# Kernel optimization log

Hardware: AMD Instinct MI355X
Metric: run time of the kernel (lower is better)

Reference implementation:

```python
import jax, jax.numpy as jnp
import numpy as np

DIST_THRESHOLD = 900.0  # distance_threshold from __init__
NO_CODE_ID = -1         # no_code_id from __init__


def setup_inputs() -> dict:
    key = jax.random.key(0)
    k1, k2 = jax.random.split(key)
    x = jax.random.normal(k1, (4, 2048, 512), dtype=jnp.float32)      # [b, n, d] tokens
    codes = jax.random.normal(k2, (16384, 512), dtype=jnp.float32)    # [c, d] full codebook
    return {"x": x, "codes": codes}


def reference(x, codes):
    x2 = jnp.sum(x * x, axis=-1, keepdims=True)            # [b, n, 1]
    c2 = jnp.sum(codes * codes, axis=-1)                   # [c]
    xc = jnp.einsum('bnd,cd->bnc', x, codes)               # [b, n, c] (the compute-heavy GEMM)
    dist_sq = jnp.maximum(x2 + c2 - 2.0 * xc, 0.0)         # clamp tiny negatives, like cdist

    within = jnp.any(dist_sq <= DIST_THRESHOLD, axis=-1)   # [b, n]
    nn_ids = jnp.argmin(dist_sq, axis=-1)                  # [b, n]
    ids = jnp.where(within, nn_ids, NO_CODE_ID)            # tokens outside threshold -> no_code_id
    return ids
```

## Files before the change

### kernel.cpp

```cpp
#include <hip/hip_runtime.h>


#define NTOK   8192
#define NCODES 16384
#define DDIM   512
#define NCHUNK 8
#define CHUNK  2048
#define DIST_THR 900.0f

typedef unsigned short u16;
typedef _Float16 half8 __attribute__((ext_vector_type(8)));
typedef float    f32x4 __attribute__((ext_vector_type(4)));

__device__ __forceinline__ void conv_body(const float* __restrict__ src,
                                          u16* __restrict__ dh,
                                          u16* __restrict__ dl, int c) {
    int r = c & 15, q = (c >> 4) & 3, g = (c >> 6) & 7, kit = (c >> 9) & 15;
    int tile = c >> 13;
    int row = tile * 128 + g * 16 + r;
    int k = kit * 32 + q * 8;
    const float* p = src + (size_t)row * DDIM + k;
    float4 v0 = *(const float4*)p;
    float4 v1 = *(const float4*)(p + 4);
    float vv[8] = {v0.x, v0.y, v0.z, v0.w, v1.x, v1.y, v1.z, v1.w};
    u16 hs[8], ls[8];
    #pragma unroll
    for (int j = 0; j < 8; ++j) {
        float sv = vv[j] * 16.0f;
        _Float16 h = (_Float16)sv;
        float hf = (float)h;
        _Float16 l = (_Float16)(sv - hf);
        union { _Float16 f; u16 u; } uh, ul;
        uh.f = h; ul.f = l;
        hs[j] = uh.u; ls[j] = ul.u;
    }
    uint4 H, L;
    H.x = hs[0] | ((unsigned)hs[1] << 16); H.y = hs[2] | ((unsigned)hs[3] << 16);
    H.z = hs[4] | ((unsigned)hs[5] << 16); H.w = hs[6] | ((unsigned)hs[7] << 16);
    L.x = ls[0] | ((unsigned)ls[1] << 16); L.y = ls[2] | ((unsigned)ls[3] << 16);
    L.z = ls[4] | ((unsigned)ls[5] << 16); L.w = ls[6] | ((unsigned)ls[7] << 16);
    *(uint4*)(dh + (size_t)c * 8) = H;
    *(uint4*)(dl + (size_t)c * 8) = L;
}

__global__ __launch_bounds__(256) void nn_prep(const float* __restrict__ x,
                                               const float* __restrict__ codes,
                                               u16* __restrict__ xh, u16* __restrict__ xl,
                                               u16* __restrict__ ch, u16* __restrict__ cl,
                                               float* __restrict__ c2) {
    int b = blockIdx.x;
    if (b < 2048) {
        conv_body(x, xh, xl, b * 256 + threadIdx.x);
    } else if (b < 6144) {
        conv_body(codes, ch, cl, (b - 2048) * 256 + threadIdx.x);
    } else {
        int w = threadIdx.x >> 6;
        int lane = threadIdx.x & 63;
        int c = (b - 6144) * 4 + w;
        const float* p = codes + (size_t)c * DDIM + lane * 8;
        float4 v0 = *(const float4*)p;
        float4 v1 = *(const float4*)(p + 4);
        float s = v0.x*v0.x + v0.y*v0.y + v0.z*v0.z + v0.w*v0.w
                + v1.x*v1.x + v1.y*v1.y + v1.z*v1.z + v1.w*v1.w;
        #pragma unroll
        for (int off = 32; off > 0; off >>= 1) s += __shfl_down(s, off);
        if (lane == 0) c2[c] = s;
    }
}

__global__ __launch_bounds__(512, 2) void nn_gemm(const u16* __restrict__ xh,
                                                  const u16* __restrict__ xl,
                                                  const u16* __restrict__ chh,
                                                  const u16* __restrict__ cll,
                                                  const float* __restrict__ c2,
                                                  float* __restrict__ pmin,
                                                  int* __restrict__ pid) {
    __shared__ __align__(16) char smem[131072];
    const int tid = threadIdx.x;
    const int lane = tid & 63;
    const int wave = tid >> 6;
    const int wm = wave & 3;
    const int wn = wave >> 2;
    const int mtile = blockIdx.x >> 3;
    const int chunk = blockIdx.x & 7;
    const int m0 = mtile * 256;

    const int plane = wave >> 1;
    const int tsub  = wave & 1;
    const bool isA = (plane < 2);
    const u16* gbase;
    if (plane == 0)      gbase = xh  + ((size_t)(mtile * 2 + tsub) * 16) * 4096;
    else if (plane == 1) gbase = xl  + ((size_t)(mtile * 2 + tsub) * 16) * 4096;
    else if (plane == 2) gbase = chh + ((size_t)(chunk * 16 + tsub) * 16) * 4096;
    else                 gbase = cll + ((size_t)(chunk * 16 + tsub) * 16) * 4096;
    gbase += lane * 8;
    const int ldsoff = wave * 8192;

    float mv[16];
    int   mi[16];
    #pragma unroll
    for (int s = 0; s < 16; ++s) { mv[s] = 3.4e38f; mi[s] = 0; }

    f32x4 acc[4][8];
    #pragma unroll
    for (int i = 0; i < 4; ++i)
        #pragma unroll
        for (int j = 0; j < 8; ++j) acc[i][j] = (f32x4)0.0f;

    auto stage = [&](int it2) {
        int kit2 = it2 & 15, nt2 = it2 >> 4;
        size_t off = (size_t)(isA ? kit2 : nt2 * 32 + kit2) * 4096;
        const u16* src = gbase + off;
        char* dst = smem + (size_t)(it2 & 1) * 65536 + ldsoff;
        #pragma unroll
        for (int s = 0; s < 8; ++s)
            __builtin_amdgcn_global_load_lds(
                (const __attribute__((address_space(1))) void*)(src + s * 512),
                (__attribute__((address_space(3))) void*)(dst + s * 1024),
                16, 0, 0);
    };

    stage(0);
    for (int it = 0; it < 128; ++it) {
        if (it < 127) {
            stage(it + 1);
            asm volatile("s_waitcnt vmcnt(8)\n\ts_barrier" ::: "memory");
        } else {
            asm volatile("s_waitcnt vmcnt(0)\n\ts_barrier" ::: "memory");
        }

        const char* cur = smem + (size_t)(it & 1) * 65536;
        half8 ah[4], al[4];
        #pragma unroll
        for (int i = 0; i < 4; ++i) {
            int g = wm * 4 + i;
            ah[i] = *(const half8*)(cur +         g * 1024 + lane * 16);
            al[i] = *(const half8*)(cur + 16384 + g * 1024 + lane * 16);
        }
        #pragma unroll
        for (int j = 0; j < 8; ++j) {
            int g = wn * 8 + j;
            half8 bh = *(const half8*)(cur + 32768 + g * 1024 + lane * 16);
            half8 bl = *(const half8*)(cur + 49152 + g * 1024 + lane * 16);
            #pragma unroll
            for (int i = 0; i < 4; ++i) {
                acc[i][j] = __builtin_amdgcn_mfma_f32_16x16x32_f16(ah[i], bh, acc[i][j], 0, 0, 0);
                acc[i][j] = __builtin_amdgcn_mfma_f32_16x16x32_f16(ah[i], bl, acc[i][j], 0, 0, 0);
                acc[i][j] = __builtin_amdgcn_mfma_f32_16x16x32_f16(al[i], bh, acc[i][j], 0, 0, 0);
            }
        }

        if ((it & 15) == 15) {
            int nt = it >> 4;
            #pragma unroll
            for (int j = 0; j < 8; ++j) {
                int ncol = nt * 256 + wn * 128 + j * 16 + (lane & 15);
                int gid = chunk * CHUNK + ncol;
                float cv = c2[gid];
                #pragma unroll
                for (int i = 0; i < 4; ++i)
                    #pragma unroll
                    for (int r = 0; r < 4; ++r) {
                        float s = fmaf(acc[i][j][r], -0.0078125f, cv);
                        int slot = i * 4 + r;
                        if (s < mv[slot]) { mv[slot] = s; mi[slot] = gid; }
                    }
            }
            #pragma unroll
            for (int i = 0; i < 4; ++i)
                #pragma unroll
                for (int j = 0; j < 8; ++j) acc[i][j] = (f32x4)0.0f;
        }
        asm volatile("s_barrier" ::: "memory");
    }

    #pragma unroll
    for (int off = 1; off < 16; off <<= 1) {
        #pragma unroll
        for (int s = 0; s < 16; ++s) {
            float ov = __shfl_xor(mv[s], off);
            int   oi = __shfl_xor(mi[s], off);
            if (ov < mv[s] || (ov == mv[s] && oi < mi[s])) { mv[s] = ov; mi[s] = oi; }
        }
    }
    if ((lane & 15) == 0) {
        #pragma unroll
        for (int i = 0; i < 4; ++i)
            #pragma unroll
            for (int r = 0; r < 4; ++r) {
                int row = wm * 64 + i * 16 + (lane >> 4) * 4 + r;
                int2 e;
                e.x = __float_as_int(mv[i * 4 + r]);
                e.y = mi[i * 4 + r];
                *(int2*)(smem + (wn * 256 + row) * 8) = e;
            }
    }
    __syncthreads();
    if (tid < 256) {
        int2 e0 = *(const int2*)(smem + tid * 8);
        int2 e1 = *(const int2*)(smem + (256 + tid) * 8);
        float v0 = __int_as_float(e0.x), v1 = __int_as_float(e1.x);
        float bv = v0; int bi = e0.y;
        if (v1 < bv || (v1 == bv && e1.y < bi)) { bv = v1; bi = e1.y; }
        pmin[(size_t)(m0 + tid) * NCHUNK + chunk] = bv;
        pid [(size_t)(m0 + tid) * NCHUNK + chunk] = bi;
    }
}

__global__ __launch_bounds__(256) void nn_fin(const float* __restrict__ x,
                                              const float* __restrict__ pmin,
                                              const int* __restrict__ pid,
                                              int* __restrict__ out) {
    int w = threadIdx.x >> 6;
    int lane = threadIdx.x & 63;
    int t = blockIdx.x * 4 + w;
    const float* p = x + (size_t)t * DDIM + lane * 8;
    float4 v0 = *(const float4*)p;
    float4 v1 = *(const float4*)(p + 4);
    float s = v0.x*v0.x + v0.y*v0.y + v0.z*v0.z + v0.w*v0.w
            + v1.x*v1.x + v1.y*v1.y + v1.z*v1.z + v1.w*v1.w;
    #pragma unroll
    for (int off = 32; off > 0; off >>= 1) s += __shfl_down(s, off);
    if (lane == 0) {
        const float* pm = pmin + (size_t)t * NCHUNK;
        const int*   pi = pid  + (size_t)t * NCHUNK;
        float bv = pm[0]; int bi = pi[0];
        #pragma unroll
        for (int c = 1; c < NCHUNK; ++c) {
            float v = pm[c]; int id = pi[c];
            if (v < bv || (v == bv && id < bi)) { bv = v; bi = id; }
        }
        float mind = s + bv;
        out[t] = (mind <= DIST_THR) ? bi : -1;
    }
}

extern "C" void kernel_launch(void* const* d_in, const int* in_sizes, int n_in,
                              void* d_out, int out_size, void* d_ws, size_t ws_size,
                              hipStream_t stream) {
    const float* x     = (const float*)d_in[0];
    const float* codes = (const float*)d_in[1];
    int* out = (int*)d_out;

    char* ws = (char*)d_ws;
    u16*   xh   = (u16*)(ws);
    u16*   xl   = (u16*)(ws + 8388608);
    u16*   chh  = (u16*)(ws + 16777216);
    u16*   cll  = (u16*)(ws + 33554432);
    float* c2   = (float*)(ws + 50331648);
    float* pmin = (float*)(ws + 50397184);
    int*   pid  = (int*)  (ws + 50659328);

    nn_prep<<<10240, 256, 0, stream>>>(x, codes, xh, xl, chh, cll, c2);
    nn_gemm<<<32 * NCHUNK, 512, 0, stream>>>(xh, xl, chh, cll, c2, pmin, pid);
    nn_fin<<<NTOK / 4, 256, 0, stream>>>(x, pmin, pid, out);
}
```

Measured before the change: 409.0 us.

## Interleave LDS reads and MFMA clusters with barriers and priority scheduling

Restructures the main K-loop so B fragments are read from LDS in pairs and each pair's MFMA cluster runs in a fenced block under raised wave priority. Waves are kept in lockstep with extra barriers. The prefetch of the next stage is issued after the first LDS reads, and the wait on the global load moves to the end of the iteration. The aim is to overlap LDS traffic and global-to-LDS loads with MFMA execution, similar to ping-pong scheduling. The cost is many more barriers per iteration, which may add synchronization stalls.

Result: no change. 406.8 us (-0.6%).

```diff
diff --git a/kernel.cpp b/kernel.cpp
--- a/kernel.cpp
+++ b/kernel.cpp
@@ -121,33 +121,63 @@
     };
 
     stage(0);
+    asm volatile("s_waitcnt vmcnt(0)\n\ts_barrier" ::: "memory");
+
     for (int it = 0; it < 128; ++it) {
-        if (it < 127) {
-            stage(it + 1);
-            asm volatile("s_waitcnt vmcnt(8)\n\ts_barrier" ::: "memory");
-        } else {
-            asm volatile("s_waitcnt vmcnt(0)\n\ts_barrier" ::: "memory");
-        }
-
         const char* cur = smem + (size_t)(it & 1) * 65536;
         half8 ah[4], al[4];
+
         #pragma unroll
         for (int i = 0; i < 4; ++i) {
             int g = wm * 4 + i;
             ah[i] = *(const half8*)(cur +         g * 1024 + lane * 16);
             al[i] = *(const half8*)(cur + 16384 + g * 1024 + lane * 16);
         }
-        #pragma unroll
-        for (int j = 0; j < 8; ++j) {
-            int g = wn * 8 + j;
-            half8 bh = *(const half8*)(cur + 32768 + g * 1024 + lane * 16);
-            half8 bl = *(const half8*)(cur + 49152 + g * 1024 + lane * 16);
+        half8 bh0 = *(const half8*)(cur + 32768 + (wn * 8 + 0) * 1024 + lane * 16);
+        half8 bl0 = *(const half8*)(cur + 49152 + (wn * 8 + 0) * 1024 + lane * 16);
+        half8 bh1 = *(const half8*)(cur + 32768 + (wn * 8 + 1) * 1024 + lane * 16);
+        half8 bl1 = *(const half8*)(cur + 49152 + (wn * 8 + 1) * 1024 + lane * 16);
+        if (it < 127) stage(it + 1);
+        asm volatile("s_barrier" ::: "memory");
+        asm volatile("s_waitcnt lgkmcnt(0)" ::: "memory");
+        __builtin_amdgcn_sched_barrier(0);
+        __builtin_amdgcn_s_setprio(1);
+        #pragma unroll
+        for (int i = 0; i < 4; ++i) {
+            acc[i][0] = __builtin_amdgcn_mfma_f32_16x16x32_f16(ah[i], bh0, acc[i][0], 0, 0, 0);
+            acc[i][0] = __builtin_amdgcn_mfma_f32_16x16x32_f16(ah[i], bl0, acc[i][0], 0, 0, 0);
+            acc[i][0] = __builtin_amdgcn_mfma_f32_16x16x32_f16(al[i], bh0, acc[i][0], 0, 0, 0);
+            acc[i][1] = __builtin_amdgcn_mfma_f32_16x16x32_f16(ah[i], bh1, acc[i][1], 0, 0, 0);
+            acc[i][1] = __builtin_amdgcn_mfma_f32_16x16x32_f16(ah[i], bl1, acc[i][1], 0, 0, 0);
+            acc[i][1] = __builtin_amdgcn_mfma_f32_16x16x32_f16(al[i], bh1, acc[i][1], 0, 0, 0);
+        }
+        __builtin_amdgcn_s_setprio(0);
+        __builtin_amdgcn_sched_barrier(0);
+        asm volatile("s_barrier" ::: "memory");
+
+        #pragma unroll
+        for (int p = 1; p < 4; ++p) {
+            const int j0 = 2 * p, j1 = 2 * p + 1;
+            half8 bhA = *(const half8*)(cur + 32768 + (wn * 8 + j0) * 1024 + lane * 16);
+            half8 blA = *(const half8*)(cur + 49152 + (wn * 8 + j0) * 1024 + lane * 16);
+            half8 bhB = *(const half8*)(cur + 32768 + (wn * 8 + j1) * 1024 + lane * 16);
+            half8 blB = *(const half8*)(cur + 49152 + (wn * 8 + j1) * 1024 + lane * 16);
+            asm volatile("s_barrier" ::: "memory");
+            asm volatile("s_waitcnt lgkmcnt(0)" ::: "memory");
+            __builtin_amdgcn_sched_barrier(0);
+            __builtin_amdgcn_s_setprio(1);
             #pragma unroll
             for (int i = 0; i < 4; ++i) {
-                acc[i][j] = __builtin_amdgcn_mfma_f32_16x16x32_f16(ah[i], bh, acc[i][j], 0, 0, 0);
-                acc[i][j] = __builtin_amdgcn_mfma_f32_16x16x32_f16(ah[i], bl, acc[i][j], 0, 0, 0);
-                acc[i][j] = __builtin_amdgcn_mfma_f32_16x16x32_f16(al[i], bh, acc[i][j], 0, 0, 0);
+                acc[i][j0] = __builtin_amdgcn_mfma_f32_16x16x32_f16(ah[i], bhA, acc[i][j0], 0, 0, 0);
+                acc[i][j0] = __builtin_amdgcn_mfma_f32_16x16x32_f16(ah[i], blA, acc[i][j0], 0, 0, 0);
+                acc[i][j0] = __builtin_amdgcn_mfma_f32_16x16x32_f16(al[i], bhA, acc[i][j0], 0, 0, 0);
+                acc[i][j1] = __builtin_amdgcn_mfma_f32_16x16x32_f16(ah[i], bhB, acc[i][j1], 0, 0, 0);
+                acc[i][j1] = __builtin_amdgcn_mfma_f32_16x16x32_f16(ah[i], blB, acc[i][j1], 0, 0, 0);
+                acc[i][j1] = __builtin_amdgcn_mfma_f32_16x16x32_f16(al[i], bhB, acc[i][j1], 0, 0, 0);
             }
+            __builtin_amdgcn_s_setprio(0);
+            __builtin_amdgcn_sched_barrier(0);
+            if (p < 3) asm volatile("s_barrier" ::: "memory");
         }
 
         if ((it & 15) == 15) {
@@ -171,7 +201,7 @@
                 #pragma unroll
                 for (int j = 0; j < 8; ++j) acc[i][j] = (f32x4)0.0f;
         }
-        asm volatile("s_barrier" ::: "memory");
+        asm volatile("s_waitcnt vmcnt(0)\n\ts_barrier" ::: "memory");
     }
 
     #pragma unroll
```

## Load A operands directly from global and stage only B through LDS

Applied to the files above, without the earlier changes.

The x tiles (A hi/lo planes) are now read by each wave straight from global memory into registers, and only the codebook tiles are staged into LDS by all eight waves. This halves shared memory per block and removes the trailing barrier per iteration, with the prefetch of the next B stage issued after the A loads. The cost is that A is re-read from global/L2 every iteration by each wave, and the barrier now waits on vmcnt(0), which exposes global latency more than the old vmcnt(8) double-buffered wait did.

After: 438.1 us. 1.07x slower.

```diff
diff --git a/kernel.cpp b/kernel.cpp
--- a/kernel.cpp
+++ b/kernel.cpp
@@ -75,7 +75,7 @@
                                                   const float* __restrict__ c2,
                                                   float* __restrict__ pmin,
                                                   int* __restrict__ pid) {
-    __shared__ __align__(16) char smem[131072];
+    __shared__ __align__(16) char smem[65536];
     const int tid = threadIdx.x;
     const int lane = tid & 63;
     const int wave = tid >> 6;
@@ -85,21 +85,22 @@
     const int chunk = blockIdx.x & 7;
     const int m0 = mtile * 256;
 
-    const int plane = wave >> 1;
-    const int tsub  = wave & 1;
-    const bool isA = (plane < 2);
-    const u16* gbase;
-    if (plane == 0)      gbase = xh  + ((size_t)(mtile * 2 + tsub) * 16) * 4096;
-    else if (plane == 1) gbase = xl  + ((size_t)(mtile * 2 + tsub) * 16) * 4096;
-    else if (plane == 2) gbase = chh + ((size_t)(chunk * 16 + tsub) * 16) * 4096;
-    else                 gbase = cll + ((size_t)(chunk * 16 + tsub) * 16) * 4096;
-    gbase += lane * 8;
-    const int ldsoff = wave * 8192;
+    const u16* abase_h = xh + (size_t)(mtile * 2 + (wm >> 1)) * 65536
+                            + (size_t)((wm & 1) * 4) * 512 + lane * 8;
+    const u16* abase_l = xl + (size_t)(mtile * 2 + (wm >> 1)) * 65536
+                            + (size_t)((wm & 1) * 4) * 512 + lane * 8;
+
+    const int q = wave >> 2;
+    const int s = wave & 3;
+    const u16* bsrc = q ? cll : chh;
+    const u16* bgbase = bsrc + (size_t)(chunk * 16 + (s >> 1)) * 65536
+                             + (size_t)(s & 1) * 2048 + lane * 8;
+    const int bldsoff = q * 16384 + (s >> 1) * 8192 + (s & 1) * 4096 + lane * 16;
 
     float mv[16];
     int   mi[16];
     #pragma unroll
-    for (int s = 0; s < 16; ++s) { mv[s] = 3.4e38f; mi[s] = 0; }
+    for (int t = 0; t < 16; ++t) { mv[t] = 3.4e38f; mi[t] = 0; }
 
     f32x4 acc[4][8];
     #pragma unroll
@@ -109,39 +110,36 @@
 
     auto stage = [&](int it2) {
         int kit2 = it2 & 15, nt2 = it2 >> 4;
-        size_t off = (size_t)(isA ? kit2 : nt2 * 32 + kit2) * 4096;
-        const u16* src = gbase + off;
-        char* dst = smem + (size_t)(it2 & 1) * 65536 + ldsoff;
-        #pragma unroll
-        for (int s = 0; s < 8; ++s)
+        const u16* src = bgbase + (size_t)nt2 * 131072 + (size_t)kit2 * 4096;
+        char* dst = smem + (it2 & 1) * 32768 + bldsoff;
+        #pragma unroll
+        for (int jj = 0; jj < 4; ++jj)
             __builtin_amdgcn_global_load_lds(
-                (const __attribute__((address_space(1))) void*)(src + s * 512),
-                (__attribute__((address_space(3))) void*)(dst + s * 1024),
+                (const __attribute__((address_space(1))) void*)(src + jj * 512),
+                (__attribute__((address_space(3))) void*)(dst + jj * 1024),
                 16, 0, 0);
     };
 
     stage(0);
     for (int it = 0; it < 128; ++it) {
-        if (it < 127) {
-            stage(it + 1);
-            asm volatile("s_waitcnt vmcnt(8)\n\ts_barrier" ::: "memory");
-        } else {
-            asm volatile("s_waitcnt vmcnt(0)\n\ts_barrier" ::: "memory");
-        }
-
-        const char* cur = smem + (size_t)(it & 1) * 65536;
+        asm volatile("s_waitcnt vmcnt(0)\n\ts_barrier" ::: "memory");
+
+        const char* cur = smem + (it & 1) * 32768;
+        const int kit = it & 15;
+
         half8 ah[4], al[4];
         #pragma unroll
         for (int i = 0; i < 4; ++i) {
-            int g = wm * 4 + i;
-            ah[i] = *(const half8*)(cur +         g * 1024 + lane * 16);
-            al[i] = *(const half8*)(cur + 16384 + g * 1024 + lane * 16);
-        }
+            ah[i] = *(const half8*)(abase_h + (size_t)kit * 4096 + i * 512);
+            al[i] = *(const half8*)(abase_l + (size_t)kit * 4096 + i * 512);
+        }
+        if (it < 127) stage(it + 1);
+
         #pragma unroll
         for (int j = 0; j < 8; ++j) {
             int g = wn * 8 + j;
-            half8 bh = *(const half8*)(cur + 32768 + g * 1024 + lane * 16);
-            half8 bl = *(const half8*)(cur + 49152 + g * 1024 + lane * 16);
+            half8 bh = *(const half8*)(cur +         g * 1024 + lane * 16);
+            half8 bl = *(const half8*)(cur + 16384 + g * 1024 + lane * 16);
             #pragma unroll
             for (int i = 0; i < 4; ++i) {
                 acc[i][j] = __builtin_amdgcn_mfma_f32_16x16x32_f16(ah[i], bh, acc[i][j], 0, 0, 0);
@@ -161,9 +159,9 @@
                 for (int i = 0; i < 4; ++i)
                     #pragma unroll
                     for (int r = 0; r < 4; ++r) {
-                        float s = fmaf(acc[i][j][r], -0.0078125f, cv);
+                        float sc = fmaf(acc[i][j][r], -0.0078125f, cv);
                         int slot = i * 4 + r;
-                        if (s < mv[slot]) { mv[slot] = s; mi[slot] = gid; }
+                        if (sc < mv[slot]) { mv[slot] = sc; mi[slot] = gid; }
                     }
             }
             #pragma unroll
@@ -171,16 +169,15 @@
                 #pragma unroll
                 for (int j = 0; j < 8; ++j) acc[i][j] = (f32x4)0.0f;
         }
-        asm volatile("s_barrier" ::: "memory");
     }
 
     #pragma unroll
     for (int off = 1; off < 16; off <<= 1) {
         #pragma unroll
-        for (int s = 0; s < 16; ++s) {
-            float ov = __shfl_xor(mv[s], off);
-            int   oi = __shfl_xor(mi[s], off);
-            if (ov < mv[s] || (ov == mv[s] && oi < mi[s])) { mv[s] = ov; mi[s] = oi; }
+        for (int t = 0; t < 16; ++t) {
+            float ov = __shfl_xor(mv[t], off);
+            int   oi = __shfl_xor(mi[t], off);
+            if (ov < mv[t] || (ov == mv[t] && oi < mi[t])) { mv[t] = ov; mi[t] = oi; }
         }
     }
     if ((lane & 15) == 0) {
```

## Switch GEMM to 32x32x16 MFMA with per-tile argmin reduction into LDS

Applied to the files above, without the earlier changes.

Replaces the 16x16x32 f16 MFMA tiling with 32x32x16 MFMA, relaying out the converted fp16 hi/lo planes so each lane feeds the larger instruction, and halves LDS fragment reads per MFMA. Because the 32x32 accumulator holds 32 row slots per lane, the running argmin no longer lives in registers. It is reduced across lanes at every N-tile boundary and merged into a new LDS table. This cuts MFMA issue and LDS traffic but adds a shuffle reduction and LDS read-modify-write per N-tile, plus extra LDS space that may affect occupancy.

New measurement: 538.2 us. 1.32x slower.

```diff
diff --git a/kernel.cpp b/kernel.cpp
--- a/kernel.cpp
+++ b/kernel.cpp
@@ -10,15 +10,17 @@
 
 typedef unsigned short u16;
 typedef _Float16 half8 __attribute__((ext_vector_type(8)));
-typedef float    f32x4 __attribute__((ext_vector_type(4)));
+typedef float    f32x4  __attribute__((ext_vector_type(4)));
+typedef float    f32x16 __attribute__((ext_vector_type(16)));
 
 __device__ __forceinline__ void conv_body(const float* __restrict__ src,
                                           u16* __restrict__ dh,
                                           u16* __restrict__ dl, int c) {
-    int r = c & 15, q = (c >> 4) & 3, g = (c >> 6) & 7, kit = (c >> 9) & 15;
+    int L = c & 63, f = (c >> 6) & 7, kit = (c >> 9) & 15;
     int tile = c >> 13;
-    int row = tile * 128 + g * 16 + r;
-    int k = kit * 32 + q * 8;
+    int g = f >> 1, ks = f & 1;
+    int row = tile * 128 + g * 32 + (L & 31);
+    int k = kit * 32 + ks * 16 + (L >> 5) * 8;
     const float* p = src + (size_t)row * DDIM + k;
     float4 v0 = *(const float4*)p;
     float4 v1 = *(const float4*)(p + 4);
@@ -30,17 +32,17 @@
         _Float16 h = (_Float16)sv;
         float hf = (float)h;
         _Float16 l = (_Float16)(sv - hf);
-        union { _Float16 f; u16 u; } uh, ul;
-        uh.f = h; ul.f = l;
+        union { _Float16 f16; u16 u; } uh, ul;
+        uh.f16 = h; ul.f16 = l;
         hs[j] = uh.u; ls[j] = ul.u;
     }
-    uint4 H, L;
-    H.x = hs[0] | ((unsigned)hs[1] << 16); H.y = hs[2] | ((unsigned)hs[3] << 16);
-    H.z = hs[4] | ((unsigned)hs[5] << 16); H.w = hs[6] | ((unsigned)hs[7] << 16);
-    L.x = ls[0] | ((unsigned)ls[1] << 16); L.y = ls[2] | ((unsigned)ls[3] << 16);
-    L.z = ls[4] | ((unsigned)ls[5] << 16); L.w = ls[6] | ((unsigned)ls[7] << 16);
+    uint4 H, Lo;
+    H.x  = hs[0] | ((unsigned)hs[1] << 16); H.y  = hs[2] | ((unsigned)hs[3] << 16);
+    H.z  = hs[4] | ((unsigned)hs[5] << 16); H.w  = hs[6] | ((unsigned)hs[7] << 16);
+    Lo.x = ls[0] | ((unsigned)ls[1] << 16); Lo.y = ls[2] | ((unsigned)ls[3] << 16);
+    Lo.z = ls[4] | ((unsigned)ls[5] << 16); Lo.w = ls[6] | ((unsigned)ls[7] << 16);
     *(uint4*)(dh + (size_t)c * 8) = H;
-    *(uint4*)(dl + (size_t)c * 8) = L;
+    *(uint4*)(dl + (size_t)c * 8) = Lo;
 }
 
 __global__ __launch_bounds__(256) void nn_prep(const float* __restrict__ x,
@@ -75,7 +77,7 @@
                                                   const float* __restrict__ c2,
                                                   float* __restrict__ pmin,
                                                   int* __restrict__ pid) {
-    __shared__ __align__(16) char smem[131072];
+    __shared__ __align__(16) char smem[139264];
     const int tid = threadIdx.x;
     const int lane = tid & 63;
     const int wave = tid >> 6;
@@ -84,6 +86,12 @@
     const int mtile = blockIdx.x >> 3;
     const int chunk = blockIdx.x & 7;
     const int m0 = mtile * 256;
+    char* tb = smem + 131072;
+
+    if (tid < 512) {
+        int2 e; e.x = __float_as_int(3.4e38f); e.y = 0;
+        *(int2*)(tb + tid * 8) = e;
+    }
 
     const int plane = wave >> 1;
     const int tsub  = wave & 1;
@@ -96,16 +104,11 @@
     gbase += lane * 8;
     const int ldsoff = wave * 8192;
 
-    float mv[16];
-    int   mi[16];
+    f32x16 acc[2][4];
     #pragma unroll
-    for (int s = 0; s < 16; ++s) { mv[s] = 3.4e38f; mi[s] = 0; }
-
-    f32x4 acc[4][8];
-    #pragma unroll
-    for (int i = 0; i < 4; ++i)
-        #pragma unroll
-        for (int j = 0; j < 8; ++j) acc[i][j] = (f32x4)0.0f;
+    for (int i = 0; i < 2; ++i)
+        #pragma unroll
+        for (int j = 0; j < 4; ++j) acc[i][j] = (f32x16)0.0f;
 
     auto stage = [&](int it2) {
         int kit2 = it2 & 15, nt2 = it2 >> 4;
@@ -130,75 +133,85 @@
         }
 
         const char* cur = smem + (size_t)(it & 1) * 65536;
-        half8 ah[4], al[4];
-        #pragma unroll
-        for (int i = 0; i < 4; ++i) {
-            int g = wm * 4 + i;
-            ah[i] = *(const half8*)(cur +         g * 1024 + lane * 16);
-            al[i] = *(const half8*)(cur + 16384 + g * 1024 + lane * 16);
-        }
-        #pragma unroll
-        for (int j = 0; j < 8; ++j) {
-            int g = wn * 8 + j;
-            half8 bh = *(const half8*)(cur + 32768 + g * 1024 + lane * 16);
-            half8 bl = *(const half8*)(cur + 49152 + g * 1024 + lane * 16);
-            #pragma unroll
-            for (int i = 0; i < 4; ++i) {
-                acc[i][j] = __builtin_amdgcn_mfma_f32_16x16x32_f16(ah[i], bh, acc[i][j], 0, 0, 0);
-                acc[i][j] = __builtin_amdgcn_mfma_f32_16x16x32_f16(ah[i], bl, acc[i][j], 0, 0, 0);
-                acc[i][j] = __builtin_amdgcn_mfma_f32_16x16x32_f16(al[i], bh, acc[i][j], 0, 0, 0);
+
+        #pragma unroll
+        for (int ks = 0; ks < 2; ++ks) {
+            half8 ah[2], al[2];
+            #pragma unroll
+            for (int i = 0; i < 2; ++i) {
+                int gg = wm * 2 + i;
+                int aoff = (gg >> 2) * 8192 + ((gg & 3) * 2 + ks) * 1024 + lane * 16;
+                ah[i] = *(const half8*)(cur +         aoff);
+                al[i] = *(const half8*)(cur + 16384 + aoff);
+            }
+            #pragma unroll
+            for (int j = 0; j < 4; ++j) {
+                int cg = wn * 4 + j;
+                int boff = 32768 + (cg >> 2) * 8192 + ((cg & 3) * 2 + ks) * 1024 + lane * 16;
+                half8 bh = *(const half8*)(cur +         boff);
+                half8 bl = *(const half8*)(cur + 16384 + boff);
+                #pragma unroll
+                for (int i = 0; i < 2; ++i) {
+                    acc[i][j] = __builtin_amdgcn_mfma_f32_32x32x16_f16(ah[i], bh, acc[i][j], 0, 0, 0);
+                    acc[i][j] = __builtin_amdgcn_mfma_f32_32x32x16_f16(ah[i], bl, acc[i][j], 0, 0, 0);
+                    acc[i][j] = __builtin_amdgcn_mfma_f32_32x32x16_f16(al[i], bh, acc[i][j], 0, 0, 0);
+                }
             }
         }
 
         if ((it & 15) == 15) {
             int nt = it >> 4;
-            #pragma unroll
-            for (int j = 0; j < 8; ++j) {
-                int ncol = nt * 256 + wn * 128 + j * 16 + (lane & 15);
-                int gid = chunk * CHUNK + ncol;
-                float cv = c2[gid];
-                #pragma unroll
-                for (int i = 0; i < 4; ++i)
+            float mvs[32]; int mis[32];
+            #pragma unroll
+            for (int s = 0; s < 32; ++s) { mvs[s] = 3.4e38f; mis[s] = 0; }
+            #pragma unroll
+            for (int j = 0; j < 4; ++j) {
+                int col = j * 32 + (lane & 31);
+                float cv = c2[chunk * CHUNK + nt * 256 + wn * 128 + col];
+                #pragma unroll
+                for (int i = 0; i < 2; ++i)
                     #pragma unroll
-                    for (int r = 0; r < 4; ++r) {
-                        float s = fmaf(acc[i][j][r], -0.0078125f, cv);
-                        int slot = i * 4 + r;
-                        if (s < mv[slot]) { mv[slot] = s; mi[slot] = gid; }
+                    for (int r = 0; r < 16; ++r) {
+                        float sc = fmaf(acc[i][j][r], -0.0078125f, cv);
+                        int slot = i * 16 + r;
+                        if (sc < mvs[slot]) { mvs[slot] = sc; mis[slot] = col; }
                     }
             }
             #pragma unroll
-            for (int i = 0; i < 4; ++i)
-                #pragma unroll
-                for (int j = 0; j < 8; ++j) acc[i][j] = (f32x4)0.0f;
+            for (int off = 1; off < 32; off <<= 1) {
+                #pragma unroll
+                for (int s = 0; s < 32; ++s) {
+                    float ov = __shfl_xor(mvs[s], off);
+                    int   oi = __shfl_xor(mis[s], off);
+                    if (ov < mvs[s] || (ov == mvs[s] && oi < mis[s])) { mvs[s] = ov; mis[s] = oi; }
+                }
+            }
+            if ((lane & 31) == 0) {
+                #pragma unroll
+                for (int s = 0; s < 32; ++s) {
+                    int row = wm * 64 + (s >> 4) * 32 + (s & 3) + ((s >> 2) & 3) * 8 + (lane >> 5) * 4;
+                    int2* e = (int2*)(tb + (wn * 256 + row) * 8);
+                    float bv = __int_as_float(e->x);
+                    if (mvs[s] < bv) {
+                        int2 w;
+                        w.x = __float_as_int(mvs[s]);
+                        w.y = chunk * CHUNK + nt * 256 + wn * 128 + mis[s];
+                        *e = w;
+                    }
+                }
+            }
+            #pragma unroll
+            for (int i = 0; i < 2; ++i)
+                #pragma unroll
+                for (int j = 0; j < 4; ++j) acc[i][j] = (f32x16)0.0f;
         }
         asm volatile("s_barrier" ::: "memory");
     }
 
-    #pragma unroll
-    for (int off = 1; off < 16; off <<= 1) {
-        #pragma unroll
-        for (int s = 0; s < 16; ++s) {
-            float ov = __shfl_xor(mv[s], off);
-            int   oi = __shfl_xor(mi[s], off);
-            if (ov < mv[s] || (ov == mv[s] && oi < mi[s])) { mv[s] = ov; mi[s] = oi; }
-        }
-    }
-    if ((lane & 15) == 0) {
-        #pragma unroll
-        for (int i = 0; i < 4; ++i)
-            #pragma unroll
-            for (int r = 0; r < 4; ++r) {
-                int row = wm * 64 + i * 16 + (lane >> 4) * 4 + r;
-                int2 e;
-                e.x = __float_as_int(mv[i * 4 + r]);
-                e.y = mi[i * 4 + r];
-                *(int2*)(smem + (wn * 256 + row) * 8) = e;
-            }
-    }
     __syncthreads();
     if (tid < 256) {
-        int2 e0 = *(const int2*)(smem + tid * 8);
-        int2 e1 = *(const int2*)(smem + (256 + tid) * 8);
+        int2 e0 = *(const int2*)(tb + tid * 8);
+        int2 e1 = *(const int2*)(tb + (256 + tid) * 8);
         float v0 = __int_as_float(e0.x), v1 = __int_as_float(e1.x);
         float bv = v0; int bi = e0.y;
         if (v1 < bv || (v1 == bv && e1.y < bi)) { bv = v1; bi = e1.y; }
```
